# Performance work log

Hardware: AMD Instinct MI355X
Metric: run time of the kernel (lower is better)

Reference implementation:

```python
import jax, jax.numpy as jnp
import numpy as np

B, S, A, H, NH = 4, 4096, 512, 1024, 16
HD = H // NH  # 64


def setup_inputs() -> dict:
    key = jax.random.key(0)
    ks = jax.random.split(key, 12)
    s = 1.0 / np.sqrt(H)
    return {
        "hidden_states": jax.random.normal(ks[0], (B, S, H), jnp.float32),
        "audio_tokens": jax.random.normal(ks[1], (B, A, H), jnp.float32),
        "attention_mask": jax.random.randint(ks[2], (B, A), 0, 2, jnp.int32),
        "Wq": jax.random.normal(ks[3], (H, H), jnp.float32) * s,
        "bq": jnp.zeros((H,), jnp.float32),
        "Wk": jax.random.normal(ks[4], (H, H), jnp.float32) * s,
        "bk": jnp.zeros((H,), jnp.float32),
        "Wv": jax.random.normal(ks[5], (H, H), jnp.float32) * s,
        "bv": jnp.zeros((H,), jnp.float32),
        "Wo": jax.random.normal(ks[6], (H, H), jnp.float32) * s,
        "bo": jnp.zeros((H,), jnp.float32),
        "ln_gamma": jnp.ones((H,), jnp.float32),
        "ln_beta": jnp.zeros((H,), jnp.float32),
        "residual_scale": jnp.asarray(0.05, jnp.float32),
    }


def _san(x, big=10000.0):
    return jnp.nan_to_num(x, nan=0.0, posinf=big, neginf=-big)


def reference(hidden_states, audio_tokens, attention_mask, Wq, bq, Wk, bk, Wv, bv,
              Wo, bo, ln_gamma, ln_beta, residual_scale):
    hs = _san(hidden_states).astype(jnp.float32)
    at = _san(audio_tokens).astype(jnp.float32)

    def heads(x, W, b):  # [b, t, H] -> [b, t, nh, hd]
        return _san(x @ W.T + b).reshape(x.shape[0], x.shape[1], NH, HD)

    q = heads(hs, Wq, bq)            # [B,S,NH,HD]
    k = heads(at, Wk, bk)            # [B,A,NH,HD]
    v = heads(at, Wv, bv)            # [B,A,NH,HD]

    scale = max(np.sqrt(HD), 1e-8)
    scores = jnp.einsum("bsnd,band->bnsa", q, k) / scale  # [B,NH,S,A]
    scores = jnp.clip(_san(jnp.clip(scores, -50.0, 50.0), 50.0), -50.0, 50.0)

    attend = (attention_mask > 0)[:, None, None, :]       # [B,1,1,A]
    scores = jnp.where(attend, scores, -10000.0)
    scores = jnp.clip(scores, -50.0, 50.0)

    probs = jax.nn.softmax(scores, axis=-1)
    probs = _san(probs, 1.0)
    probs = probs / (jnp.sum(probs, axis=-1, keepdims=True) + 1e-8)

    ctx = jnp.einsum("bnsa,band->bsnd", probs, v).reshape(B, S, H)
    delta = _san(ctx @ Wo.T + bo)

    rs = jnp.clip(residual_scale, 0.0, 0.3)
    delta = rs * delta

    mu = jnp.mean(delta, axis=-1, keepdims=True)
    var = jnp.mean(jnp.square(delta - mu), axis=-1, keepdims=True)
    delta = (delta - mu) / jnp.sqrt(var + 1e-5) * ln_gamma + ln_beta
    return delta
```

## Files before the change

### kernel.cpp

```cpp
#include <hip/hip_runtime.h>
#include <hip/hip_bf16.h>
#include <cstdint>
#include <cstddef>

#define B_  4
#define S_  4096
#define A_  512
#define H_  1024
#define NH_ 16
#define HD_ 64

typedef __bf16 bf16;
typedef __bf16 bf16x8 __attribute__((ext_vector_type(8)));
typedef __bf16 bf16x4 __attribute__((ext_vector_type(4)));
typedef float  fx4    __attribute__((ext_vector_type(4)));

typedef __attribute__((address_space(3))) void LDS_v;
typedef const __attribute__((address_space(1))) void GLB_v;

__device__ __forceinline__ void gl_lds16(const void* g, void* l) {
    __builtin_amdgcn_global_load_lds((GLB_v*)g, (LDS_v*)l, 16, 0, 0);
}

__device__ __forceinline__ float sanf(float x) {
    if (x != x) return 0.f;
    if (fabsf(x) == __builtin_inff()) return x > 0.f ? 10000.f : -10000.f;
    return x;
}

__global__ __launch_bounds__(256) void cast_all(const float* __restrict__ hs,
                                                const float* __restrict__ at,
                                                const float* __restrict__ wq,
                                                const float* __restrict__ wk,
                                                const float* __restrict__ wv,
                                                const float* __restrict__ wo,
                                                bf16* __restrict__ dhs, bf16* __restrict__ dat,
                                                bf16* __restrict__ dwq, bf16* __restrict__ dwk,
                                                bf16* __restrict__ dwv, bf16* __restrict__ dwo) {
    int i = blockIdx.x * 256 + threadIdx.x;
    const float* s; bf16* d; int off;
    if (i < 4194304)      { s = hs; d = dhs; off = i; }
    else if (i < 4718592) { s = at; d = dat; off = i - 4194304; }
    else if (i < 4980736) { s = wq; d = dwq; off = i - 4718592; }
    else if (i < 5242880) { s = wk; d = dwk; off = i - 4980736; }
    else if (i < 5505024) { s = wv; d = dwv; off = i - 5242880; }
    else                  { s = wo; d = dwo; off = i - 5505024; }
    float4 v = ((const float4*)s)[off];
    bf16x4 o;
    o[0] = (bf16)sanf(v.x); o[1] = (bf16)sanf(v.y);
    o[2] = (bf16)sanf(v.z); o[3] = (bf16)sanf(v.w);
    *(bf16x4*)&d[(size_t)off * 4] = o;
}

__global__ __launch_bounds__(256) void qkv_gemm(const bf16* __restrict__ hsb,
                                                const bf16* __restrict__ atb,
                                                const bf16* __restrict__ wqb,
                                                const bf16* __restrict__ wkb,
                                                const bf16* __restrict__ wvb,
                                                const float* __restrict__ bq,
                                                const float* __restrict__ bk,
                                                const float* __restrict__ bv,
                                                bf16* __restrict__ Qb,
                                                bf16* __restrict__ Kb,
                                                bf16* __restrict__ Vtb) {
    __shared__ __align__(16) bf16 As[128 * 32];
    __shared__ __align__(16) bf16 Bs[128 * 32];

    const int id = blockIdx.x;
    int mode, m0, n0;
    const bf16 *A, *Bt; const float* bias;
    if (id < 1024)      { mode = 0; m0 = (id & 127) * 128; n0 = (id >> 7) * 128; A = hsb; Bt = wqb; bias = bq; }
    else if (id < 1152) { int t = id - 1024; mode = 1; m0 = (t & 15) * 128; n0 = (t >> 4) * 128; A = atb; Bt = wkb; bias = bk; }
    else                { int t = id - 1152; mode = 2; m0 = (t & 15) * 128; n0 = (t >> 4) * 128; A = atb; Bt = wvb; bias = bv; }

    const int tid  = threadIdx.x;
    const int lane = tid & 63;
    const int wv   = tid >> 6;
    const int wr   = wv >> 1, wc = wv & 1;
    const int lr   = lane & 15, kq = lane >> 4;

    fx4 acc[4][4] = {};

    const bf16* Ag = A  + (size_t)m0 * 1024;
    const bf16* Bg = Bt + (size_t)n0 * 1024;
    const int c0 = tid, c1 = tid + 256;
    const int row0 = c0 >> 2, kc0 = c0 & 3;
    const int row1 = c1 >> 2, kc1 = c1 & 3;

    for (int k0 = 0; k0 < 1024; k0 += 32) {
        gl_lds16(Ag + (size_t)row0 * 1024 + k0 + kc0 * 8, &As[c0 * 8]);
        gl_lds16(Ag + (size_t)row1 * 1024 + k0 + kc1 * 8, &As[c1 * 8]);
        gl_lds16(Bg + (size_t)row0 * 1024 + k0 + kc0 * 8, &Bs[c0 * 8]);
        gl_lds16(Bg + (size_t)row1 * 1024 + k0 + kc1 * 8, &Bs[c1 * 8]);
        __syncthreads();
        bf16x8 af[4], bfr[4];
#pragma unroll
        for (int i = 0; i < 4; i++) af[i]  = *(const bf16x8*)&As[(wr * 64 + i * 16 + lr) * 32 + kq * 8];
#pragma unroll
        for (int j = 0; j < 4; j++) bfr[j] = *(const bf16x8*)&Bs[(wc * 64 + j * 16 + lr) * 32 + kq * 8];
#pragma unroll
        for (int i = 0; i < 4; i++)
#pragma unroll
            for (int j = 0; j < 4; j++)
                acc[i][j] = __builtin_amdgcn_mfma_f32_16x16x32_bf16(af[i], bfr[j], acc[i][j], 0, 0, 0);
        __syncthreads();
    }

    float bb[4];
#pragma unroll
    for (int j = 0; j < 4; j++) bb[j] = bias[n0 + wc * 64 + j * 16 + lr];

    if (mode == 0) {
        const float sc = 0.18033688011112042f;
#pragma unroll
        for (int i = 0; i < 4; i++) {
            int row = m0 + wr * 64 + i * 16 + kq * 4;
#pragma unroll
            for (int j = 0; j < 4; j++) {
                int col = n0 + wc * 64 + j * 16 + lr;
#pragma unroll
                for (int r = 0; r < 4; r++)
                    Qb[(size_t)(row + r) * 1024 + col] = (bf16)((acc[i][j][r] + bb[j]) * sc);
            }
        }
    } else if (mode == 1) {
#pragma unroll
        for (int i = 0; i < 4; i++) {
            int row = m0 + wr * 64 + i * 16 + kq * 4;
#pragma unroll
            for (int j = 0; j < 4; j++) {
                int col = n0 + wc * 64 + j * 16 + lr;
#pragma unroll
                for (int r = 0; r < 4; r++)
                    Kb[(size_t)(row + r) * 1024 + col] = (bf16)(acc[i][j][r] + bb[j]);
            }
        }
    } else {
#pragma unroll
        for (int i = 0; i < 4; i++) {
            int m = m0 + wr * 64 + i * 16 + kq * 4;
            int bidx = m >> 9, a = m & 511;
#pragma unroll
            for (int j = 0; j < 4; j++) {
                int col = n0 + wc * 64 + j * 16 + lr;
                bf16x4 o;
#pragma unroll
                for (int r = 0; r < 4; r++) o[r] = (bf16)(acc[i][j][r] + bb[j]);
                *(bf16x4*)&Vtb[((size_t)bidx * H_ + col) * A_ + a] = o;
            }
        }
    }
}

__global__ __launch_bounds__(256) void gemm_o(const bf16* __restrict__ A,
                                              const bf16* __restrict__ Bt,
                                              const float* __restrict__ bias,
                                              bf16* __restrict__ C,
                                              const float* __restrict__ rsp) {
    __shared__ __align__(16) bf16 As[128 * 32];
    __shared__ __align__(16) bf16 Bs[128 * 32];

    const int tid  = threadIdx.x;
    const int lane = tid & 63;
    const int wv   = tid >> 6;
    const int wr   = wv >> 1, wc = wv & 1;
    const int lr   = lane & 15, kq = lane >> 4;
    const int m0   = blockIdx.x * 128, n0 = blockIdx.y * 128;

    fx4 acc[4][4] = {};

    const bf16* Ag = A  + (size_t)m0 * 1024;
    const bf16* Bg = Bt + (size_t)n0 * 1024;
    const int c0 = tid, c1 = tid + 256;
    const int row0 = c0 >> 2, kc0 = c0 & 3;
    const int row1 = c1 >> 2, kc1 = c1 & 3;

    for (int k0 = 0; k0 < 1024; k0 += 32) {
        gl_lds16(Ag + (size_t)row0 * 1024 + k0 + kc0 * 8, &As[c0 * 8]);
        gl_lds16(Ag + (size_t)row1 * 1024 + k0 + kc1 * 8, &As[c1 * 8]);
        gl_lds16(Bg + (size_t)row0 * 1024 + k0 + kc0 * 8, &Bs[c0 * 8]);
        gl_lds16(Bg + (size_t)row1 * 1024 + k0 + kc1 * 8, &Bs[c1 * 8]);
        __syncthreads();
        bf16x8 af[4], bfr[4];
#pragma unroll
        for (int i = 0; i < 4; i++) af[i]  = *(const bf16x8*)&As[(wr * 64 + i * 16 + lr) * 32 + kq * 8];
#pragma unroll
        for (int j = 0; j < 4; j++) bfr[j] = *(const bf16x8*)&Bs[(wc * 64 + j * 16 + lr) * 32 + kq * 8];
#pragma unroll
        for (int i = 0; i < 4; i++)
#pragma unroll
            for (int j = 0; j < 4; j++)
                acc[i][j] = __builtin_amdgcn_mfma_f32_16x16x32_bf16(af[i], bfr[j], acc[i][j], 0, 0, 0);
        __syncthreads();
    }

    float bb[4];
#pragma unroll
    for (int j = 0; j < 4; j++) bb[j] = bias[n0 + wc * 64 + j * 16 + lr];
    float rs = fminf(fmaxf(rsp[0], 0.f), 0.3f);
#pragma unroll
    for (int i = 0; i < 4; i++) {
        int row = m0 + wr * 64 + i * 16 + kq * 4;
#pragma unroll
        for (int j = 0; j < 4; j++) {
            int col = n0 + wc * 64 + j * 16 + lr;
#pragma unroll
            for (int r = 0; r < 4; r++)
                C[(size_t)(row + r) * 1024 + col] = (bf16)(rs * (acc[i][j][r] + bb[j]));
        }
    }
}

__global__ __launch_bounds__(256, 4) void attn_kernel(const bf16* __restrict__ Q,
                                                      const bf16* __restrict__ Kb,
                                                      const bf16* __restrict__ Vt,
                                                      const int* __restrict__ mask,
                                                      bf16* __restrict__ ctx) {
    __shared__ __align__(16) bf16 Qs[128 * 72];
    __shared__ __align__(16) bf16 Ks[64 * 72];
    __shared__ __align__(16) bf16 Vts[64 * 72];
    __shared__ float smask[512];
    __shared__ float dnm[128];

    const int tid  = threadIdx.x;
    const int lane = tid & 63;
    const int wv   = tid >> 6;
    const int lr   = lane & 15, kq = lane >> 4;
    const int st = blockIdx.x, h = blockIdx.y, b = blockIdx.z;
    const int m0 = b * S_ + st * 128;
    const float LO = -72.134752f;

    bf16x8 qtmp[4];
#pragma unroll
    for (int i = 0; i < 4; i++) {
        int c = tid + i * 256, row = c >> 3, ch = c & 7;
        qtmp[i] = *(const bf16x8*)(Q + (size_t)(m0 + row) * H_ + h * 64 + ch * 8);
    }
    smask[tid]       = (mask[b * A_ + tid] > 0)       ? -LO : LO;
    smask[tid + 256] = (mask[b * A_ + tid + 256] > 0) ? -LO : LO;
#pragma unroll
    for (int i = 0; i < 4; i++) {
        int c = tid + i * 256, row = c >> 3, ch = c & 7;
        *(bf16x8*)&Qs[row * 72 + ch * 8] = qtmp[i];
    }

    const int srow = tid >> 2, sseg = tid & 3;
    const size_t kg = (size_t)(b * A_ + srow) * H_ + h * 64 + sseg * 16;
    const bf16* vrow = Vt + (size_t)(b * H_ + h * 64 + srow) * A_;
    const int va0 = 32 * (sseg >> 1) + 4 * ((2 * sseg) & 3);
    const int va1 = 32 * (sseg >> 1) + 4 * ((2 * sseg + 1) & 3);

    bf16x8 kr0 = *(const bf16x8*)(Kb + kg);
    bf16x8 kr1 = *(const bf16x8*)(Kb + kg + 8);
    bf16x4 v00 = *(const bf16x4*)(vrow + va0);
    bf16x4 v01 = *(const bf16x4*)(vrow + va0 + 16);
    bf16x4 v10 = *(const bf16x4*)(vrow + va1);
    bf16x4 v11 = *(const bf16x4*)(vrow + va1 + 16);

    fx4 acco[2][4] = {};
    float dloc[2] = {0.f, 0.f};

    for (int it = 0; it < 8; it++) {
        const int a0 = it * 64;
        __syncthreads();
        *(bf16x8*)&Ks[srow * 72 + sseg * 16]      = kr0;
        *(bf16x8*)&Ks[srow * 72 + sseg * 16 + 8]  = kr1;
        *(bf16x8*)&Vts[srow * 72 + sseg * 16] =
            __builtin_shufflevector(v00, v01, 0, 1, 2, 3, 4, 5, 6, 7);
        *(bf16x8*)&Vts[srow * 72 + sseg * 16 + 8] =
            __builtin_shufflevector(v10, v11, 0, 1, 2, 3, 4, 5, 6, 7);
        __syncthreads();

        if (it < 7) {
            const size_t ko = kg + (size_t)(a0 + 64) * H_;
            kr0 = *(const bf16x8*)(Kb + ko);
            kr1 = *(const bf16x8*)(Kb + ko + 8);
            v00 = *(const bf16x4*)(vrow + a0 + 64 + va0);
            v01 = *(const bf16x4*)(vrow + a0 + 64 + va0 + 16);
            v10 = *(const bf16x4*)(vrow + a0 + 64 + va1);
            v11 = *(const bf16x4*)(vrow + a0 + 64 + va1 + 16);
        }

        fx4 accs[4][2] = {};
#pragma unroll
        for (int kk = 0; kk < 64; kk += 32) {
            bf16x8 kf[4], qf[2];
#pragma unroll
            for (int mt = 0; mt < 4; mt++)
                kf[mt] = *(const bf16x8*)&Ks[(mt * 16 + lr) * 72 + kk + kq * 8];
#pragma unroll
            for (int nt = 0; nt < 2; nt++)
                qf[nt] = *(const bf16x8*)&Qs[(wv * 32 + nt * 16 + lr) * 72 + kk + kq * 8];
#pragma unroll
            for (int mt = 0; mt < 4; mt++)
#pragma unroll
                for (int nt = 0; nt < 2; nt++)
                    accs[mt][nt] = __builtin_amdgcn_mfma_f32_16x16x32_bf16(kf[mt], qf[nt], accs[mt][nt], 0, 0, 0);
        }

        bf16x4 pf[4][2];
#pragma unroll
        for (int mt = 0; mt < 4; mt++) {
            fx4 cap = *(const fx4*)&smask[a0 + mt * 16 + kq * 4];
#pragma unroll
            for (int nt = 0; nt < 2; nt++) {
#pragma unroll
                for (int r = 0; r < 4; r++) {
                    float s2 = fmaxf(fminf(accs[mt][nt][r], cap[r]), LO);
                    float p  = __builtin_amdgcn_exp2f(s2);
                    pf[mt][nt][r] = (bf16)p;
                    dloc[nt] += p;
                }
            }
        }

#pragma unroll
        for (int ks = 0; ks < 2; ks++) {
            bf16x8 pa[2];
#pragma unroll
            for (int stl = 0; stl < 2; stl++)
                pa[stl] = __builtin_shufflevector(pf[2 * ks][stl], pf[2 * ks + 1][stl],
                                                  0, 1, 2, 3, 4, 5, 6, 7);
#pragma unroll
            for (int dt = 0; dt < 4; dt++) {
                bf16x8 vf = *(const bf16x8*)&Vts[(dt * 16 + lr) * 72 + ks * 32 + kq * 8];
#pragma unroll
                for (int stl = 0; stl < 2; stl++)
                    acco[stl][dt] = __builtin_amdgcn_mfma_f32_16x16x32_bf16(pa[stl], vf, acco[stl][dt], 0, 0, 0);
            }
        }
    }

#pragma unroll
    for (int nt = 0; nt < 2; nt++) {
        dloc[nt] += __shfl_xor(dloc[nt], 16);
        dloc[nt] += __shfl_xor(dloc[nt], 32);
    }
    if (kq == 0) {
        dnm[wv * 32 + lr]      = dloc[0];
        dnm[wv * 32 + 16 + lr] = dloc[1];
    }
    __syncthreads();

#pragma unroll
    for (int stl = 0; stl < 2; stl++) {
        fx4 dv = *(const fx4*)&dnm[wv * 32 + stl * 16 + kq * 4];
        float ri[4];
#pragma unroll
        for (int r = 0; r < 4; r++) ri[r] = __builtin_amdgcn_rcpf(dv[r]);
#pragma unroll
        for (int dt = 0; dt < 4; dt++)
#pragma unroll
            for (int r = 0; r < 4; r++)
                Qs[(wv * 32 + stl * 16 + kq * 4 + r) * 72 + dt * 16 + lr] =
                    (bf16)(acco[stl][dt][r] * ri[r]);
    }
    __syncthreads();
#pragma unroll
    for (int i = 0; i < 4; i++) {
        int c = tid + i * 256, row = c >> 3, ch = c & 7;
        *(bf16x8*)&ctx[(size_t)(m0 + row) * H_ + h * 64 + ch * 8] = *(const bf16x8*)&Qs[row * 72 + ch * 8];
    }
}

__global__ __launch_bounds__(256) void ln_kernel(const bf16* __restrict__ in,
                                                 float* __restrict__ out,
                                                 const float* __restrict__ gamma,
                                                 const float* __restrict__ beta) {
    __shared__ float red[8];
    const int tid = threadIdx.x;
    bf16x4 xb = *(const bf16x4*)&in[(size_t)blockIdx.x * 1024 + tid * 4];
    float x0 = (float)xb[0], x1 = (float)xb[1], x2 = (float)xb[2], x3 = (float)xb[3];
    float s = x0 + x1 + x2 + x3;
    float q = x0 * x0 + x1 * x1 + x2 * x2 + x3 * x3;
#pragma unroll
    for (int off = 32; off > 0; off >>= 1) {
        s += __shfl_down(s, off);
        q += __shfl_down(q, off);
    }
    if ((tid & 63) == 0) { red[(tid >> 6) * 2] = s; red[(tid >> 6) * 2 + 1] = q; }
    __syncthreads();
    s = red[0] + red[2] + red[4] + red[6];
    q = red[1] + red[3] + red[5] + red[7];
    float mean = s * (1.f / 1024.f);
    float var  = q * (1.f / 1024.f) - mean * mean;
    float inv  = rsqrtf(var + 1e-5f);
    float4 g  = ((const float4*)gamma)[tid];
    float4 bb = ((const float4*)beta)[tid];
    float4 y;
    y.x = (x0 - mean) * inv * g.x + bb.x;
    y.y = (x1 - mean) * inv * g.y + bb.y;
    y.z = (x2 - mean) * inv * g.z + bb.z;
    y.w = (x3 - mean) * inv * g.w + bb.w;
    ((float4*)(out + (size_t)blockIdx.x * 1024))[tid] = y;
}

extern "C" void kernel_launch(void* const* d_in, const int* in_sizes, int n_in,
                              void* d_out, int out_size, void* d_ws, size_t ws_size,
                              hipStream_t stream) {
    const float* hs    = (const float*)d_in[0];
    const float* at    = (const float*)d_in[1];
    const int*   maskp = (const int*)d_in[2];
    const float* Wq    = (const float*)d_in[3];
    const float* bq    = (const float*)d_in[4];
    const float* Wk    = (const float*)d_in[5];
    const float* bk    = (const float*)d_in[6];
    const float* Wv    = (const float*)d_in[7];
    const float* bv    = (const float*)d_in[8];
    const float* Wo    = (const float*)d_in[9];
    const float* bo    = (const float*)d_in[10];
    const float* gamma = (const float*)d_in[11];
    const float* beta  = (const float*)d_in[12];
    const float* rsp   = (const float*)d_in[13];

    char* ws = (char*)d_ws;
    bf16* hsb = (bf16*)(ws + 0);
    bf16* ctx = (bf16*)(ws + 0);
    bf16* atb = (bf16*)(ws + 33554432);
    bf16* wqb = (bf16*)(ws + 37748736);
    bf16* wkb = (bf16*)(ws + 39845888);
    bf16* wvb = (bf16*)(ws + 41943040);
    bf16* wob = (bf16*)(ws + 44040192);
    bf16* Qb  = (bf16*)(ws + 46137344);
    bf16* Ob  = Qb;
    bf16* Kb  = (bf16*)(ws + 79691776);
    bf16* Vtb = (bf16*)(ws + 83886080);

    cast_all<<<22528, 256, 0, stream>>>(hs, at, Wq, Wk, Wv, Wo,
                                        hsb, atb, wqb, wkb, wvb, wob);

    qkv_gemm<<<1280, 256, 0, stream>>>(hsb, atb, wqb, wkb, wvb,
                                       bq, bk, bv, Qb, Kb, Vtb);

    attn_kernel<<<dim3(32, 16, 4), 256, 0, stream>>>(Qb, Kb, Vtb, maskp, ctx);

    gemm_o<<<dim3(128, 8), 256, 0, stream>>>(ctx, wob, bo, Ob, rsp);
    ln_kernel<<<16384, 256, 0, stream>>>(Ob, (float*)d_out, gamma, beta);
}
```

Baseline: 327.5 us.

## Transpose GEMM MFMA operands for vector stores; compute softmax denominator via MFMA

For the Q/K and output projections, the MFMA operand order is swapped so each lane holds four consecutive output columns. The epilogue can then write bf16x4 vectors and load bias as float4 instead of doing scattered scalar stores. In attention, the per-row softmax sum is computed by an extra MFMA against a ones vector, replacing VALU accumulation, cross-lane shuffles and an LDS round trip. The clamp is also folded into a single fmed3. The denominator now sums the bf16-rounded probabilities, which changes numerics slightly and adds MFMA work.

```diff
diff --git a/kernel.cpp b/kernel.cpp
--- a/kernel.cpp
+++ b/kernel.cpp
@@ -98,44 +98,26 @@
         for (int i = 0; i < 4; i++) af[i]  = *(const bf16x8*)&As[(wr * 64 + i * 16 + lr) * 32 + kq * 8];
 #pragma unroll
         for (int j = 0; j < 4; j++) bfr[j] = *(const bf16x8*)&Bs[(wc * 64 + j * 16 + lr) * 32 + kq * 8];
-#pragma unroll
-        for (int i = 0; i < 4; i++)
-#pragma unroll
-            for (int j = 0; j < 4; j++)
-                acc[i][j] = __builtin_amdgcn_mfma_f32_16x16x32_bf16(af[i], bfr[j], acc[i][j], 0, 0, 0);
-        __syncthreads();
-    }
-
-    float bb[4];
-#pragma unroll
-    for (int j = 0; j < 4; j++) bb[j] = bias[n0 + wc * 64 + j * 16 + lr];
-
-    if (mode == 0) {
-        const float sc = 0.18033688011112042f;
-#pragma unroll
-        for (int i = 0; i < 4; i++) {
-            int row = m0 + wr * 64 + i * 16 + kq * 4;
-#pragma unroll
-            for (int j = 0; j < 4; j++) {
-                int col = n0 + wc * 64 + j * 16 + lr;
-#pragma unroll
-                for (int r = 0; r < 4; r++)
-                    Qb[(size_t)(row + r) * 1024 + col] = (bf16)((acc[i][j][r] + bb[j]) * sc);
-            }
-        }
-    } else if (mode == 1) {
-#pragma unroll
-        for (int i = 0; i < 4; i++) {
-            int row = m0 + wr * 64 + i * 16 + kq * 4;
-#pragma unroll
-            for (int j = 0; j < 4; j++) {
-                int col = n0 + wc * 64 + j * 16 + lr;
-#pragma unroll
-                for (int r = 0; r < 4; r++)
-                    Kb[(size_t)(row + r) * 1024 + col] = (bf16)(acc[i][j][r] + bb[j]);
-            }
-        }
-    } else {
+        if (mode == 2) {
+#pragma unroll
+            for (int i = 0; i < 4; i++)
+#pragma unroll
+                for (int j = 0; j < 4; j++)
+                    acc[i][j] = __builtin_amdgcn_mfma_f32_16x16x32_bf16(af[i], bfr[j], acc[i][j], 0, 0, 0);
+        } else {
+#pragma unroll
+            for (int i = 0; i < 4; i++)
+#pragma unroll
+                for (int j = 0; j < 4; j++)
+                    acc[i][j] = __builtin_amdgcn_mfma_f32_16x16x32_bf16(bfr[i], af[j], acc[i][j], 0, 0, 0);
+        }
+        __syncthreads();
+    }
+
+    if (mode == 2) {
+        float bb[4];
+#pragma unroll
+        for (int j = 0; j < 4; j++) bb[j] = bias[n0 + wc * 64 + j * 16 + lr];
 #pragma unroll
         for (int i = 0; i < 4; i++) {
             int m = m0 + wr * 64 + i * 16 + kq * 4;
@@ -147,6 +129,24 @@
 #pragma unroll
                 for (int r = 0; r < 4; r++) o[r] = (bf16)(acc[i][j][r] + bb[j]);
                 *(bf16x4*)&Vtb[((size_t)bidx * H_ + col) * A_ + a] = o;
+            }
+        }
+    } else {
+        const float sc = (mode == 0) ? 0.18033688011112042f : 1.0f;
+        bf16* outp = (mode == 0) ? Qb : Kb;
+        fx4 bb4[4];
+#pragma unroll
+        for (int i = 0; i < 4; i++) bb4[i] = *(const fx4*)&bias[n0 + wc * 64 + i * 16 + kq * 4];
+#pragma unroll
+        for (int i = 0; i < 4; i++) {
+            int n = n0 + wc * 64 + i * 16 + kq * 4;
+#pragma unroll
+            for (int j = 0; j < 4; j++) {
+                int m = m0 + wr * 64 + j * 16 + lr;
+                bf16x4 o;
+#pragma unroll
+                for (int r = 0; r < 4; r++) o[r] = (bf16)((acc[i][j][r] + bb4[i][r]) * sc);
+                *(bf16x4*)&outp[(size_t)m * 1024 + n] = o;
             }
         }
     }
@@ -190,23 +190,24 @@
         for (int i = 0; i < 4; i++)
 #pragma unroll
             for (int j = 0; j < 4; j++)
-                acc[i][j] = __builtin_amdgcn_mfma_f32_16x16x32_bf16(af[i], bfr[j], acc[i][j], 0, 0, 0);
-        __syncthreads();
-    }
-
-    float bb[4];
-#pragma unroll
-    for (int j = 0; j < 4; j++) bb[j] = bias[n0 + wc * 64 + j * 16 + lr];
+                acc[i][j] = __builtin_amdgcn_mfma_f32_16x16x32_bf16(bfr[i], af[j], acc[i][j], 0, 0, 0);
+        __syncthreads();
+    }
+
     float rs = fminf(fmaxf(rsp[0], 0.f), 0.3f);
+    fx4 bb4[4];
+#pragma unroll
+    for (int i = 0; i < 4; i++) bb4[i] = *(const fx4*)&bias[n0 + wc * 64 + i * 16 + kq * 4];
 #pragma unroll
     for (int i = 0; i < 4; i++) {
-        int row = m0 + wr * 64 + i * 16 + kq * 4;
+        int n = n0 + wc * 64 + i * 16 + kq * 4;
 #pragma unroll
         for (int j = 0; j < 4; j++) {
-            int col = n0 + wc * 64 + j * 16 + lr;
-#pragma unroll
-            for (int r = 0; r < 4; r++)
-                C[(size_t)(row + r) * 1024 + col] = (bf16)(rs * (acc[i][j][r] + bb[j]));
+            int m = m0 + wr * 64 + j * 16 + lr;
+            bf16x4 o;
+#pragma unroll
+            for (int r = 0; r < 4; r++) o[r] = (bf16)(rs * (acc[i][j][r] + bb4[i][r]));
+            *(bf16x4*)&C[(size_t)m * 1024 + n] = o;
         }
     }
 }
@@ -220,7 +221,6 @@
     __shared__ __align__(16) bf16 Ks[64 * 72];
     __shared__ __align__(16) bf16 Vts[64 * 72];
     __shared__ float smask[512];
-    __shared__ float dnm[128];
 
     const int tid  = threadIdx.x;
     const int lane = tid & 63;
@@ -258,7 +258,10 @@
     bf16x4 v11 = *(const bf16x4*)(vrow + va1 + 16);
 
     fx4 acco[2][4] = {};
-    float dloc[2] = {0.f, 0.f};
+    fx4 dacc[2]    = {};
+    bf16x8 ones8;
+#pragma unroll
+    for (int e = 0; e < 8; e++) ones8[e] = (bf16)1.0f;
 
     for (int it = 0; it < 8; it++) {
         const int a0 = it * 64;
@@ -306,10 +309,8 @@
             for (int nt = 0; nt < 2; nt++) {
 #pragma unroll
                 for (int r = 0; r < 4; r++) {
-                    float s2 = fmaxf(fminf(accs[mt][nt][r], cap[r]), LO);
-                    float p  = __builtin_amdgcn_exp2f(s2);
-                    pf[mt][nt][r] = (bf16)p;
-                    dloc[nt] += p;
+                    float s2 = __builtin_amdgcn_fmed3f(accs[mt][nt][r], LO, cap[r]);
+                    pf[mt][nt][r] = (bf16)__builtin_amdgcn_exp2f(s2);
                 }
             }
         }
@@ -328,26 +329,19 @@
                 for (int stl = 0; stl < 2; stl++)
                     acco[stl][dt] = __builtin_amdgcn_mfma_f32_16x16x32_bf16(pa[stl], vf, acco[stl][dt], 0, 0, 0);
             }
-        }
-    }
-
-#pragma unroll
-    for (int nt = 0; nt < 2; nt++) {
-        dloc[nt] += __shfl_xor(dloc[nt], 16);
-        dloc[nt] += __shfl_xor(dloc[nt], 32);
-    }
-    if (kq == 0) {
-        dnm[wv * 32 + lr]      = dloc[0];
-        dnm[wv * 32 + 16 + lr] = dloc[1];
-    }
+#pragma unroll
+            for (int stl = 0; stl < 2; stl++)
+                dacc[stl] = __builtin_amdgcn_mfma_f32_16x16x32_bf16(pa[stl], ones8, dacc[stl], 0, 0, 0);
+        }
+    }
+
     __syncthreads();
 
 #pragma unroll
     for (int stl = 0; stl < 2; stl++) {
-        fx4 dv = *(const fx4*)&dnm[wv * 32 + stl * 16 + kq * 4];
         float ri[4];
 #pragma unroll
-        for (int r = 0; r < 4; r++) ri[r] = __builtin_amdgcn_rcpf(dv[r]);
+        for (int r = 0; r < 4; r++) ri[r] = __builtin_amdgcn_rcpf(dacc[stl][r]);
 #pragma unroll
         for (int dt = 0; dt < 4; dt++)
 #pragma unroll
```

After: 374.1 us. 1.14x slower.
